# Optimization experiments

Measured on AMD Instinct MI355X. Metric: run time of the kernel, lower is better.

## Reference

```python
import jax, jax.numpy as jnp
import numpy as np

N = 50000      # nodes
E = 500000     # edges (before self-loops)
IN_CH = 16     # input feature channels (x has 2 pos cols + IN_CH)
HID = 16       # hidden_channels


def _spatial_conv(x, pos, src, dst, W_in, b_in, W_out, b_out, n_nodes):
    # src/dst already include self-loops. x: [n_nodes, C], pos: [n_nodes, 2]
    C = x.shape[1]
    rel = pos[src] - pos[dst]                                  # [E', 2]
    s = jax.nn.relu(rel @ W_in + b_in)                         # [E', HID*C]
    # dropout(p=0.1) is identity in eval mode
    xj = x[src]                                                # [E', C]
    m = (s.reshape(-1, s.shape[1] // C, C) * xj[:, None, :]).reshape(s.shape)
    agg = jax.ops.segment_sum(m, dst, num_segments=n_nodes)   # [n_nodes, HID*C]
    return agg @ W_out + b_out                                 # [n_nodes, HID]


def setup_inputs() -> dict:
    key = jax.random.key(0)
    ks = jax.random.split(key, 16)
    d = {}
    d["x"] = jax.random.normal(ks[0], (N, 2 + IN_CH), dtype=jnp.float32)
    d["edge_index"] = jax.random.randint(ks[1], (2, E), 0, N, dtype=jnp.int32)
    dims = [(IN_CH, HID), (HID, HID), (HID, HID)]
    for l, (ci, h) in enumerate(dims, 1):
        d[f"W_in{l}"] = jax.random.normal(ks[2 * l], (2, h * ci), dtype=jnp.float32) * 0.1
        d[f"b_in{l}"] = jnp.zeros((h * ci,), jnp.float32)
        d[f"W_out{l}"] = jax.random.normal(ks[2 * l + 1], (h * ci, HID), dtype=jnp.float32) * 0.1
        d[f"b_out{l}"] = jnp.zeros((HID,), jnp.float32)
    d["Wd1"] = jax.random.normal(ks[8], (2 * HID, HID), dtype=jnp.float32) * 0.1
    d["bd1"] = jnp.zeros((HID,), jnp.float32)
    d["Wd2"] = jax.random.normal(ks[9], (HID, HID), dtype=jnp.float32) * 0.1
    d["bd2"] = jnp.zeros((HID,), jnp.float32)
    d["Wd3"] = jax.random.normal(ks[10], (HID, 1), dtype=jnp.float32) * 0.1
    d["bd3"] = jnp.zeros((1,), jnp.float32)
    return d


def reference(x, edge_index, W_in1, b_in1, W_out1, b_out1,
              W_in2, b_in2, W_out2, b_out2,
              W_in3, b_in3, W_out3, b_out3,
              Wd1, bd1, Wd2, bd2, Wd3, bd3):
    n = x.shape[0]
    pos = x[:, :2]
    feat = x[:, 2:]
    # add self-loops for message passing (PyG add_self_loops)
    loops = jnp.arange(n, dtype=edge_index.dtype)
    src = jnp.concatenate([edge_index[0], loops])
    dst = jnp.concatenate([edge_index[1], loops])
    h = _spatial_conv(feat, pos, src, dst, W_in1, b_in1, W_out1, b_out1, n)
    h = _spatial_conv(h, pos, src, dst, W_in2, b_in2, W_out2, b_out2, n)
    h = _spatial_conv(h, pos, src, dst, W_in3, b_in3, W_out3, b_out3, n)
    # decoder on original edge_index (no self-loops)
    z = jnp.concatenate([h[edge_index[0]], h[edge_index[1]]], axis=-1)  # [E, 2*HID]
    z = jax.nn.relu(z @ Wd1 + bd1)
    z = jax.nn.relu(z @ Wd2 + bd2)
    z = jax.nn.sigmoid(z @ Wd3 + bd3)
    return z.reshape(-1)  # [E]
```

## Files before the change

### kernel.cpp

```cpp
#include <hip/hip_runtime.h>
#include <math.h>


struct WPtrs {
    const float* bin0; const float* wout0;
    const float* bin1; const float* wout1;
    const float* bin2; const float* wout2;
};

__global__ __launch_bounds__(256) void prep_kernel(
    const float* __restrict__ x, float* __restrict__ pos,
    float* __restrict__ feat, int n)
{
    int i = blockIdx.x * 256 + threadIdx.x;
    if (i >= n) return;
    const float* r = x + (size_t)i * 18;
    float2 p; p.x = r[0]; p.y = r[1];
    ((float2*)pos)[i] = p;
    float4* fp = (float4*)feat + (size_t)i * 4;
    fp[0] = make_float4(r[2],  r[3],  r[4],  r[5]);
    fp[1] = make_float4(r[6],  r[7],  r[8],  r[9]);
    fp[2] = make_float4(r[10], r[11], r[12], r[13]);
    fp[3] = make_float4(r[14], r[15], r[16], r[17]);
}

__global__ __launch_bounds__(256) void zero_kernel(int* __restrict__ p, int* __restrict__ total, int n)
{
    int i = blockIdx.x * 256 + threadIdx.x;
    if (i < n) p[i] = 0;
    if (i == 0) *total = 0;
}

__global__ __launch_bounds__(256) void hist_kernel(
    const int* __restrict__ ei, int* __restrict__ counts, int E)
{
    int e = blockIdx.x * 256 + threadIdx.x;
    if (e < E) atomicAdd(&counts[ei[E + e]], 1);
}

__global__ __launch_bounds__(256) void reserve_kernel(
    const int* __restrict__ counts, int* __restrict__ start,
    int* __restrict__ cursor, int* __restrict__ total, int n)
{
    __shared__ int sdata[256];
    __shared__ int sbase;
    int t = threadIdx.x;
    int i = blockIdx.x * 256 + t;
    int c = (i < n) ? counts[i] : 0;
    sdata[t] = c;
    __syncthreads();
    #pragma unroll
    for (int off = 1; off < 256; off <<= 1) {
        int v = (t >= off) ? sdata[t - off] : 0;
        __syncthreads();
        sdata[t] += v;
        __syncthreads();
    }
    if (t == 255) sbase = atomicAdd(total, sdata[255]);
    __syncthreads();
    if (i < n) {
        int s = sbase + sdata[t] - c;
        start[i]  = s;
        cursor[i] = s;
    }
}

__global__ __launch_bounds__(256) void scatter_kernel(
    const int* __restrict__ ei, const float* __restrict__ pos,
    int* __restrict__ cursor, int* __restrict__ ssrc,
    float2* __restrict__ srel, int E)
{
    int e = blockIdx.x * 256 + threadIdx.x;
    if (e >= E) return;
    int s = ei[e];
    int d = ei[E + e];
    int p = atomicAdd(&cursor[d], 1);
    ssrc[p] = s;
    float2 ps = ((const float2*)pos)[s];
    float2 pd = ((const float2*)pos)[d];
    srel[p] = make_float2(ps.x - pd.x, ps.y - pd.y);
}

__global__ __launch_bounds__(256) void wself_kernel(WPtrs wp, float* __restrict__ wself)
{
    int l = blockIdx.x;
    const float* bin  = (l == 0) ? wp.bin0  : (l == 1) ? wp.bin1  : wp.bin2;
    const float* wout = (l == 0) ? wp.wout0 : (l == 1) ? wp.wout1 : wp.wout2;
    int t = threadIdx.x;
    int c = t >> 4, o = t & 15;
    float acc = 0.f;
    #pragma unroll
    for (int h = 0; h < 16; ++h) {
        int hc = h * 16 + c;
        acc += fmaxf(bin[hc], 0.f) * wout[hc * 16 + o];
    }
    wself[l * 256 + t] = acc;
}

__global__ __launch_bounds__(256) void edge_contrib_kernel(
    const int* __restrict__ ssrc,
    const float2* __restrict__ srel,
    const float* __restrict__ fin,
    const float* __restrict__ Win,
    const float* __restrict__ bin,
    const float* __restrict__ Wout,
    float* __restrict__ contrib,
    int E)
{
    int p = blockIdx.x * 256 + threadIdx.x;
    bool valid = (p < E);
    int pp = valid ? p : 0;
    int s = ssrc[pp];
    float2 r = srel[pp];

    const float4* fp = (const float4*)fin + (size_t)s * 4;
    float4 a = fp[0], b = fp[1], c4 = fp[2], d4 = fp[3];
    float xj[16] = { a.x,a.y,a.z,a.w, b.x,b.y,b.z,b.w,
                     c4.x,c4.y,c4.z,c4.w, d4.x,d4.y,d4.z,d4.w };

    float acc[16];
    #pragma unroll
    for (int o = 0; o < 16; ++o) acc[o] = 0.f;

    #pragma unroll 1
    for (int h = 0; h < 16; ++h) {
        #pragma unroll
        for (int c = 0; c < 16; ++c) {
            int hc = h * 16 + c;
            float sv = fmaf(r.x, Win[hc], fmaf(r.y, Win[256 + hc], bin[hc]));
            sv = fmaxf(sv, 0.f);
            float t = sv * xj[c];
            const float* wr = Wout + hc * 16;
            #pragma unroll
            for (int o = 0; o < 16; ++o)
                acc[o] = fmaf(t, wr[o], acc[o]);
        }
    }

    if (valid) {
        float4* op = (float4*)(contrib + (size_t)p * 16);
        op[0] = make_float4(acc[0],  acc[1],  acc[2],  acc[3]);
        op[1] = make_float4(acc[4],  acc[5],  acc[6],  acc[7]);
        op[2] = make_float4(acc[8],  acc[9],  acc[10], acc[11]);
        op[3] = make_float4(acc[12], acc[13], acc[14], acc[15]);
    }
}

__global__ __launch_bounds__(256) void segsum_kernel(
    const int* __restrict__ start, const int* __restrict__ counts,
    const float* __restrict__ contrib,
    const float* __restrict__ fin, const float* __restrict__ wself,
    const float* __restrict__ bout, float* __restrict__ out, int n)
{
    int tid = blockIdx.x * 256 + threadIdx.x;
    int node = tid >> 2;
    int q = tid & 3;
    if (node >= n) return;

    const float4* ip = (const float4*)fin + (size_t)node * 4;
    float4 f0 = ip[0], f1 = ip[1], f2 = ip[2], f3 = ip[3];
    float xin[16] = { f0.x,f0.y,f0.z,f0.w, f1.x,f1.y,f1.z,f1.w,
                      f2.x,f2.y,f2.z,f2.w, f3.x,f3.y,f3.z,f3.w };

    float4 acc = ((const float4*)bout)[q];
    #pragma unroll
    for (int c = 0; c < 16; ++c) {
        float t = xin[c];
        float4 w = ((const float4*)wself)[c * 4 + q];
        acc.x = fmaf(t, w.x, acc.x);
        acc.y = fmaf(t, w.y, acc.y);
        acc.z = fmaf(t, w.z, acc.z);
        acc.w = fmaf(t, w.w, acc.w);
    }

    int b = start[node];
    int e = b + counts[node];
    for (int k = b; k < e; ++k) {
        float4 v = ((const float4*)contrib)[(size_t)k * 4 + q];
        acc.x += v.x; acc.y += v.y; acc.z += v.z; acc.w += v.w;
    }

    ((float4*)(out + (size_t)node * 16))[q] = acc;
}

__global__ __launch_bounds__(256) void decode_kernel(
    const int* __restrict__ ei, const float* __restrict__ h,
    const float* __restrict__ Wd1, const float* __restrict__ bd1,
    const float* __restrict__ Wd2, const float* __restrict__ bd2,
    const float* __restrict__ Wd3, const float* __restrict__ bd3,
    float* __restrict__ out, int E)
{
    int tid = blockIdx.x * 256 + threadIdx.x;
    bool valid = (tid < E);
    int e = valid ? tid : 0;
    int s = ei[e];
    int d = ei[E + e];

    const float4* hp = (const float4*)h + (size_t)s * 4;
    float4 a = hp[0], b = hp[1], c4 = hp[2], d4 = hp[3];
    float hs[16] = { a.x,a.y,a.z,a.w, b.x,b.y,b.z,b.w,
                     c4.x,c4.y,c4.z,c4.w, d4.x,d4.y,d4.z,d4.w };
    const float4* hq = (const float4*)h + (size_t)d * 4;
    float4 e0 = hq[0], e1 = hq[1], e2 = hq[2], e3 = hq[3];
    float hd[16] = { e0.x,e0.y,e0.z,e0.w, e1.x,e1.y,e1.z,e1.w,
                     e2.x,e2.y,e2.z,e2.w, e3.x,e3.y,e3.z,e3.w };

    float z1[16];
    #pragma unroll
    for (int o = 0; o < 16; ++o) z1[o] = bd1[o];
    #pragma unroll
    for (int c = 0; c < 16; ++c) {
        float u = hs[c], v = hd[c];
        #pragma unroll
        for (int o = 0; o < 16; ++o)
            z1[o] = fmaf(u, Wd1[c * 16 + o], fmaf(v, Wd1[(16 + c) * 16 + o], z1[o]));
    }

    float z2[16];
    #pragma unroll
    for (int o = 0; o < 16; ++o) z2[o] = bd2[o];
    #pragma unroll
    for (int c = 0; c < 16; ++c) {
        float t = fmaxf(z1[c], 0.f);
        #pragma unroll
        for (int o = 0; o < 16; ++o)
            z2[o] = fmaf(t, Wd2[c * 16 + o], z2[o]);
    }

    float y = bd3[0];
    #pragma unroll
    for (int c = 0; c < 16; ++c)
        y = fmaf(fmaxf(z2[c], 0.f), Wd3[c], y);

    if (valid)
        out[tid] = 1.f / (1.f + expf(-y));
}

extern "C" void kernel_launch(void* const* d_in, const int* in_sizes, int n_in,
                              void* d_out, int out_size, void* d_ws, size_t ws_size,
                              hipStream_t stream)
{
    const float* x     = (const float*)d_in[0];
    const int*   ei    = (const int*)  d_in[1];
    const float* Win1  = (const float*)d_in[2];
    const float* bin1  = (const float*)d_in[3];
    const float* Wout1 = (const float*)d_in[4];
    const float* bout1 = (const float*)d_in[5];
    const float* Win2  = (const float*)d_in[6];
    const float* bin2  = (const float*)d_in[7];
    const float* Wout2 = (const float*)d_in[8];
    const float* bout2 = (const float*)d_in[9];
    const float* Win3  = (const float*)d_in[10];
    const float* bin3  = (const float*)d_in[11];
    const float* Wout3 = (const float*)d_in[12];
    const float* bout3 = (const float*)d_in[13];
    const float* Wd1   = (const float*)d_in[14];
    const float* bd1   = (const float*)d_in[15];
    const float* Wd2   = (const float*)d_in[16];
    const float* bd2   = (const float*)d_in[17];
    const float* Wd3   = (const float*)d_in[18];
    const float* bd3   = (const float*)d_in[19];

    int n = in_sizes[0] / 18;
    int E = in_sizes[1] / 2;

    float* ws      = (float*)d_ws;
    float* pos     = ws;
    float* feat    = pos   + (size_t)2 * n;
    float* hA      = feat  + (size_t)16 * n;
    float* hB      = hA    + (size_t)16 * n;
    float* wself   = hB    + (size_t)16 * n;
    int* counts    = (int*)(wself + 768);
    int* start     = counts + n;
    int* cursor    = start + n;
    int* total     = cursor + n;
    int* ssrc      = total + 2;
    float2* srel   = (float2*)(ssrc + E);
    float* contrib = (float*)(srel + E);
    float* outp    = (float*)d_out;

    int nb_n  = (n + 255) / 256;
    int nb_e  = (E + 255) / 256;
    int nb_s  = (4 * n + 255) / 256;

    prep_kernel<<<nb_n, 256, 0, stream>>>(x, pos, feat, n);
    zero_kernel<<<nb_n, 256, 0, stream>>>(counts, total, n);
    hist_kernel<<<nb_e, 256, 0, stream>>>(ei, counts, E);
    reserve_kernel<<<nb_n, 256, 0, stream>>>(counts, start, cursor, total, n);
    scatter_kernel<<<nb_e, 256, 0, stream>>>(ei, pos, cursor, ssrc, srel, E);

    WPtrs wp { bin1, Wout1, bin2, Wout2, bin3, Wout3 };
    wself_kernel<<<3, 256, 0, stream>>>(wp, wself);

    edge_contrib_kernel<<<nb_e, 256, 0, stream>>>(ssrc, srel, feat, Win1, bin1, Wout1, contrib, E);
    segsum_kernel<<<nb_s, 256, 0, stream>>>(start, counts, contrib, feat, wself + 0,   bout1, hA, n);
    edge_contrib_kernel<<<nb_e, 256, 0, stream>>>(ssrc, srel, hA,   Win2, bin2, Wout2, contrib, E);
    segsum_kernel<<<nb_s, 256, 0, stream>>>(start, counts, contrib, hA,   wself + 256, bout2, hB, n);
    edge_contrib_kernel<<<nb_e, 256, 0, stream>>>(ssrc, srel, hB,   Win3, bin3, Wout3, contrib, E);
    segsum_kernel<<<nb_s, 256, 0, stream>>>(start, counts, contrib, hB,   wself + 512, bout3, hA, n);

    decode_kernel<<<nb_e, 256, 0, stream>>>(ei, hA, Wd1, bd1, Wd2, bd2, Wd3, bd3,
                                            outp, E);
}
```

Before: 370.4 us.

## Compute per-edge message projection with split-bf16 MFMA instead of scalar FMAs

Replaces the per-thread scalar edge_contrib kernel, which does 256x16 FMAs per edge, with a wavefront-level kernel. Each wave handles 16 edges and runs the 256-wide contraction against W_out on 16x16x32 bf16 MFMA instructions. To keep near-fp32 accuracy, both the edge activations and the weights are split into hi and lo bf16 parts, and three MFMA products (HH, LH, HL) are accumulated. A small wsplit kernel pre-packs W_out into the MFMA B-operand layout. The cost is extra conversion work and some precision loss compared with full fp32.

```diff
diff --git a/kernel.cpp b/kernel.cpp
--- a/kernel.cpp
+++ b/kernel.cpp
@@ -1,12 +1,21 @@
 #include <hip/hip_runtime.h>
 #include <math.h>
 
+
+typedef __attribute__((ext_vector_type(8))) short bf16x8;
+typedef __attribute__((ext_vector_type(4))) float f32x4;
 
 struct WPtrs {
     const float* bin0; const float* wout0;
     const float* bin1; const float* wout1;
     const float* bin2; const float* wout2;
 };
+
+__device__ __forceinline__ unsigned cvtpk_bf16(float a, float b) {
+    unsigned r;
+    asm("v_cvt_pk_bf16_f32 %0, %1, %2" : "=v"(r) : "v"(a), "v"(b));
+    return r;
+}
 
 __global__ __launch_bounds__(256) void prep_kernel(
     const float* __restrict__ x, float* __restrict__ pos,
@@ -97,52 +106,94 @@
     wself[l * 256 + t] = acc;
 }
 
-__global__ __launch_bounds__(256) void edge_contrib_kernel(
-    const int* __restrict__ ssrc,
-    const float2* __restrict__ srel,
-    const float* __restrict__ fin,
-    const float* __restrict__ Win,
-    const float* __restrict__ bin,
-    const float* __restrict__ Wout,
-    float* __restrict__ contrib,
-    int E)
-{
-    int p = blockIdx.x * 256 + threadIdx.x;
-    bool valid = (p < E);
-    int pp = valid ? p : 0;
-    int s = ssrc[pp];
-    float2 r = srel[pp];
-
-    const float4* fp = (const float4*)fin + (size_t)s * 4;
-    float4 a = fp[0], b = fp[1], c4 = fp[2], d4 = fp[3];
-    float xj[16] = { a.x,a.y,a.z,a.w, b.x,b.y,b.z,b.w,
-                     c4.x,c4.y,c4.z,c4.w, d4.x,d4.y,d4.z,d4.w };
-
-    float acc[16];
-    #pragma unroll
-    for (int o = 0; o < 16; ++o) acc[o] = 0.f;
-
-    #pragma unroll 1
-    for (int h = 0; h < 16; ++h) {
+__global__ __launch_bounds__(256) void wsplit_kernel(WPtrs wp, unsigned* __restrict__ bsplit)
+{
+    int l = blockIdx.x;
+    const float* wout = (l == 0) ? wp.wout0 : (l == 1) ? wp.wout1 : wp.wout2;
+    int tid = threadIdx.x;
+    int lane = tid & 63;
+    int j = tid >> 6;
+    int o = lane & 15, q = lane >> 4;
+    for (int kb = 0; kb < 8; ++kb) {
+        int k0 = kb * 32 + q * 8 + 2 * j;
+        float v0 = wout[k0 * 16 + o];
+        float v1 = wout[(k0 + 1) * 16 + o];
+        unsigned hp = cvtpk_bf16(v0, v1);
+        float h0 = __uint_as_float(hp << 16);
+        float h1 = __uint_as_float(hp & 0xFFFF0000u);
+        unsigned lp = cvtpk_bf16(v0 - h0, v1 - h1);
+        int base = ((l * 2 + 0) * 8 + kb) * 256 + lane * 4 + j;
+        bsplit[base] = hp;
+        bsplit[base + 8 * 256] = lp;
+    }
+}
+
+__global__ __launch_bounds__(256) void edge_mfma_kernel(
+    const int* __restrict__ ssrc, const float2* __restrict__ srel,
+    const float* __restrict__ fin, const float* __restrict__ Win,
+    const float* __restrict__ bin, const unsigned* __restrict__ bsplit,
+    float* __restrict__ contrib, int E)
+{
+    int wid  = (blockIdx.x * 256 + threadIdx.x) >> 6;
+    int lane = threadIdx.x & 63;
+    int g16  = wid * 16;
+    int er   = lane & 15;
+    int q    = lane >> 4;
+    int e    = min(g16 + er, E - 1);
+    int src  = ssrc[e];
+    float2 r = srel[e];
+
+    int c0 = (q & 1) * 8;
+    const float4* fx = (const float4*)(fin + (size_t)src * 16 + c0);
+    float4 xa = fx[0], xb = fx[1];
+    float xj[8] = {xa.x, xa.y, xa.z, xa.w, xb.x, xb.y, xb.z, xb.w};
+
+    f32x4 accHH = {0.f,0.f,0.f,0.f};
+    f32x4 accLH = {0.f,0.f,0.f,0.f};
+    f32x4 accHL = {0.f,0.f,0.f,0.f};
+
+    #pragma unroll 2
+    for (int kb = 0; kb < 8; ++kb) {
+        int gk0 = kb * 32 + q * 8;
+        const float4* p1 = (const float4*)(Win + gk0);
+        const float4* p2 = (const float4*)(Win + 256 + gk0);
+        const float4* pb = (const float4*)(bin + gk0);
+        float4 w1a = p1[0], w1b = p1[1];
+        float4 w2a = p2[0], w2b = p2[1];
+        float4 bba = pb[0], bbb = pb[1];
+        float w1[8] = {w1a.x,w1a.y,w1a.z,w1a.w, w1b.x,w1b.y,w1b.z,w1b.w};
+        float w2[8] = {w2a.x,w2a.y,w2a.z,w2a.w, w2b.x,w2b.y,w2b.z,w2b.w};
+        float bv[8] = {bba.x,bba.y,bba.z,bba.w, bbb.x,bbb.y,bbb.z,bbb.w};
+
+        union { unsigned u[4]; bf16x8 v; } Ah, Al;
         #pragma unroll
-        for (int c = 0; c < 16; ++c) {
-            int hc = h * 16 + c;
-            float sv = fmaf(r.x, Win[hc], fmaf(r.y, Win[256 + hc], bin[hc]));
-            sv = fmaxf(sv, 0.f);
-            float t = sv * xj[c];
-            const float* wr = Wout + hc * 16;
-            #pragma unroll
-            for (int o = 0; o < 16; ++o)
-                acc[o] = fmaf(t, wr[o], acc[o]);
+        for (int jj = 0; jj < 4; ++jj) {
+            float t0 = fmaf(r.x, w1[2*jj],   fmaf(r.y, w2[2*jj],   bv[2*jj]));
+            float t1 = fmaf(r.x, w1[2*jj+1], fmaf(r.y, w2[2*jj+1], bv[2*jj+1]));
+            t0 = fmaxf(t0, 0.f) * xj[2*jj];
+            t1 = fmaxf(t1, 0.f) * xj[2*jj+1];
+            unsigned hp = cvtpk_bf16(t0, t1);
+            float h0 = __uint_as_float(hp << 16);
+            float h1 = __uint_as_float(hp & 0xFFFF0000u);
+            Ah.u[jj] = hp;
+            Al.u[jj] = cvtpk_bf16(t0 - h0, t1 - h1);
         }
-    }
-
-    if (valid) {
-        float4* op = (float4*)(contrib + (size_t)p * 16);
-        op[0] = make_float4(acc[0],  acc[1],  acc[2],  acc[3]);
-        op[1] = make_float4(acc[4],  acc[5],  acc[6],  acc[7]);
-        op[2] = make_float4(acc[8],  acc[9],  acc[10], acc[11]);
-        op[3] = make_float4(acc[12], acc[13], acc[14], acc[15]);
+
+        union { float4 f; bf16x8 v; } Bh, Bl;
+        Bh.f = ((const float4*)bsplit)[kb * 64 + lane];
+        Bl.f = ((const float4*)(bsplit + 2048))[kb * 64 + lane];
+
+        accHH = __builtin_amdgcn_mfma_f32_16x16x32_bf16(Ah.v, Bh.v, accHH, 0, 0, 0);
+        accLH = __builtin_amdgcn_mfma_f32_16x16x32_bf16(Al.v, Bh.v, accLH, 0, 0, 0);
+        accHL = __builtin_amdgcn_mfma_f32_16x16x32_bf16(Ah.v, Bl.v, accHL, 0, 0, 0);
+    }
+
+    f32x4 acc = accHH + accLH + accHL;
+    #pragma unroll
+    for (int rr = 0; rr < 4; ++rr) {
+        int erow = g16 + q * 4 + rr;
+        if (erow < E)
+            contrib[(size_t)erow * 16 + er] = acc[rr];
     }
 }
 
@@ -264,24 +315,26 @@
     int n = in_sizes[0] / 18;
     int E = in_sizes[1] / 2;
 
-    float* ws      = (float*)d_ws;
-    float* pos     = ws;
-    float* feat    = pos   + (size_t)2 * n;
-    float* hA      = feat  + (size_t)16 * n;
-    float* hB      = hA    + (size_t)16 * n;
-    float* wself   = hB    + (size_t)16 * n;
-    int* counts    = (int*)(wself + 768);
-    int* start     = counts + n;
-    int* cursor    = start + n;
-    int* total     = cursor + n;
-    int* ssrc      = total + 2;
-    float2* srel   = (float2*)(ssrc + E);
-    float* contrib = (float*)(srel + E);
-    float* outp    = (float*)d_out;
-
-    int nb_n  = (n + 255) / 256;
-    int nb_e  = (E + 255) / 256;
-    int nb_s  = (4 * n + 255) / 256;
+    float* ws        = (float*)d_ws;
+    float* pos       = ws;
+    float* feat      = pos   + (size_t)2 * n;
+    float* hA        = feat  + (size_t)16 * n;
+    float* hB        = hA    + (size_t)16 * n;
+    float* wself     = hB    + (size_t)16 * n;
+    unsigned* bsplit = (unsigned*)(wself + 768);
+    int* counts      = (int*)(bsplit + 12288);
+    int* start       = counts + n;
+    int* cursor      = start + n;
+    int* total       = cursor + n;
+    int* ssrc        = total + 4;
+    float2* srel     = (float2*)(ssrc + E);
+    float* contrib   = (float*)(srel + E);
+    float* outp      = (float*)d_out;
+
+    int nb_n = (n + 255) / 256;
+    int nb_e = (E + 255) / 256;
+    int nb_s = (4 * n + 255) / 256;
+    int nb_m = (E + 63) / 64;
 
     prep_kernel<<<nb_n, 256, 0, stream>>>(x, pos, feat, n);
     zero_kernel<<<nb_n, 256, 0, stream>>>(counts, total, n);
@@ -291,12 +344,16 @@
 
     WPtrs wp { bin1, Wout1, bin2, Wout2, bin3, Wout3 };
     wself_kernel<<<3, 256, 0, stream>>>(wp, wself);
-
-    edge_contrib_kernel<<<nb_e, 256, 0, stream>>>(ssrc, srel, feat, Win1, bin1, Wout1, contrib, E);
+    wsplit_kernel<<<3, 256, 0, stream>>>(wp, bsplit);
+
+    edge_mfma_kernel<<<nb_m, 256, 0, stream>>>(ssrc, srel, feat, Win1, bin1,
+                                               bsplit + 0,    contrib, E);
     segsum_kernel<<<nb_s, 256, 0, stream>>>(start, counts, contrib, feat, wself + 0,   bout1, hA, n);
-    edge_contrib_kernel<<<nb_e, 256, 0, stream>>>(ssrc, srel, hA,   Win2, bin2, Wout2, contrib, E);
+    edge_mfma_kernel<<<nb_m, 256, 0, stream>>>(ssrc, srel, hA,   Win2, bin2,
+                                               bsplit + 4096, contrib, E);
     segsum_kernel<<<nb_s, 256, 0, stream>>>(start, counts, contrib, hA,   wself + 256, bout2, hB, n);
-    edge_contrib_kernel<<<nb_e, 256, 0, stream>>>(ssrc, srel, hB,   Win3, bin3, Wout3, contrib, E);
+    edge_mfma_kernel<<<nb_m, 256, 0, stream>>>(ssrc, srel, hB,   Win3, bin3,
+                                               bsplit + 8192, contrib, E);
     segsum_kernel<<<nb_s, 256, 0, stream>>>(start, counts, contrib, hB,   wself + 512, bout3, hA, n);
 
     decode_kernel<<<nb_e, 256, 0, stream>>>(ei, hA, Wd1, bd1, Wd2, bd2, Wd3, bd3,
```

After: 414.6 us. 11.9% more time.
